# Kernel optimization log

Hardware: AMD Instinct MI355X
Metric: run time of the kernel (lower is better)

Reference implementation:

```python
import jax, jax.numpy as jnp
import numpy as np

ID, HD, B, T = 128, 256, 512, 128
MAX_REAL = 64
CAT_SEGS = [(64, 72), (72, 88), (88, 128)]
OUT_DIM = 128  # max index_end


def _lstm_scan(x, Wi, bi, Wh, bh):
    # x: [B, T, ID] -> hidden states [B, T, HD]
    b = x.shape[0]
    hd = Wh.shape[0]

    def step(carry, xt):
        h, c = carry
        gates = xt @ Wi + bi + h @ Wh + bh  # [B, 4*HD]
        f, i, a, o = jnp.split(gates, 4, axis=-1)
        f = jax.nn.sigmoid(f)
        i = jax.nn.sigmoid(i)
        a = jnp.tanh(a)
        o = jax.nn.sigmoid(o)
        c = f * c + i * a
        h = o * jnp.tanh(c)
        return (h, c), h

    init = (jnp.zeros((b, hd), x.dtype), jnp.zeros((b, hd), x.dtype))
    _, hs = jax.lax.scan(step, init, jnp.swapaxes(x, 0, 1))  # hs: [T, B, HD]
    return jnp.swapaxes(hs, 0, 1)


def setup_inputs() -> dict:
    key = jax.random.key(0)
    ks = jax.random.split(key, 16)
    s = 0.05
    inp = {
        "x0": jax.random.normal(ks[0], (B, T, ID), jnp.float32),
        "Wi_f": jax.random.normal(ks[1], (ID, 4 * HD), jnp.float32) * s,
        "bi_f": jnp.zeros((4 * HD,), jnp.float32),
        "Wh_f": jax.random.normal(ks[2], (HD, 4 * HD), jnp.float32) * s,
        "bh_f": jnp.zeros((4 * HD,), jnp.float32),
        "Wi_r": jax.random.normal(ks[3], (ID, 4 * HD), jnp.float32) * s,
        "bi_r": jnp.zeros((4 * HD,), jnp.float32),
        "Wh_r": jax.random.normal(ks[4], (HD, 4 * HD), jnp.float32) * s,
        "bh_r": jnp.zeros((4 * HD,), jnp.float32),
        "W1": jax.random.normal(ks[5], (2 * HD, HD), jnp.float32) * s,
        "b1": jnp.zeros((HD,), jnp.float32),
        "W2": jax.random.normal(ks[6], (HD, HD), jnp.float32) * s,
        "b2": jnp.zeros((HD,), jnp.float32),
        "W3": jax.random.normal(ks[7], (HD, OUT_DIM), jnp.float32) * s,
        "b3": jnp.zeros((OUT_DIM,), jnp.float32),
    }
    return inp


def reference(x0, Wi_f, bi_f, Wh_f, bh_f, Wi_r, bi_r, Wh_r, bh_r, W1, b1, W2, b2, W3, b3):
    x1_f = _lstm_scan(x0, Wi_f, bi_f, Wh_f, bh_f)            # [B, T, HD]
    x1_r = _lstm_scan(x0[:, ::-1, :], Wi_r, bi_r, Wh_r, bh_r) # [B, T, HD] (not flipped back, as in torch code)
    x1 = jnp.concatenate([x1_f, x1_r], axis=2)                # [B, T, 2*HD]
    x2 = jax.nn.leaky_relu(x1 @ W1 + b1, 0.1)
    x3 = jax.nn.leaky_relu(x2 @ W2 + b2, 0.1)
    x4 = x3 @ W3 + b3                                         # [B, T, OUT_DIM]
    parts = [jax.nn.sigmoid(x4[..., 0:MAX_REAL])]
    for s0, s1 in CAT_SEGS:
        parts.append(jax.nn.softmax(x4[..., s0:s1], axis=-1))
    return jnp.concatenate(parts, axis=-1)
```

## Files before the change

kernel.cpp:

```cpp
#include <hip/hip_runtime.h>

typedef unsigned short u16;
typedef unsigned long long u64;
typedef unsigned u32x4_t __attribute__((ext_vector_type(4)));
typedef _Float16 f16x8_t __attribute__((ext_vector_type(8)));
typedef short    i16x8_t __attribute__((ext_vector_type(8)));
typedef float    f32x4_t __attribute__((ext_vector_type(4)));

#define PIN(x) asm volatile("" : "+v"(x))

static __device__ __forceinline__ u16 f2h(float f) {
  _Float16 h = (_Float16)f;
  return __builtin_bit_cast(u16, h);
}
static __device__ __forceinline__ f32x4_t mfma16h(i16x8_t a, i16x8_t b, f32x4_t c) {
  return __builtin_amdgcn_mfma_f32_16x16x32_f16(
      __builtin_bit_cast(f16x8_t, a), __builtin_bit_cast(f16x8_t, b), c, 0, 0, 0);
}
static __device__ __forceinline__ float sigmoidf_(float x) { return 1.f / (1.f + __expf(-x)); }
static __device__ __forceinline__ float tanhf_(float x) { return 1.f - 2.f / (__expf(2.f * x) + 1.f); }

static __device__ __forceinline__ bool no_sent(u64 v) {
  u64 x = v ^ 0x7FFF7FFF7FFF7FFFull;
  return (((x - 0x0001000100010001ull) & ~x & 0x8000800080008000ull) == 0);
}
static __device__ __forceinline__ bool ok16(u32x4_t v) {
  u64 a = ((u64)v[1] << 32) | v[0];
  u64 b = ((u64)v[3] << 32) | v[2];
  return no_sent(a) && no_sent(b);
}

static __device__ __forceinline__ u32x4_t llc_load16(const u32x4_t* p) {
  u32x4_t r;
  asm volatile("global_load_dwordx4 %0, %1, off sc0 sc1\n\t"
               "s_waitcnt vmcnt(0)"
               : "=&v"(r) : "v"(p) : "memory");
  return r;
}
static __device__ __forceinline__ void llc_store4(unsigned* p, unsigned v) {
  asm volatile("global_store_dword %0, %1, off sc0 sc1" :: "v"(p), "v"(v) : "memory");
}

__global__ __launch_bounds__(256) void prep_all(
    const float* __restrict__ Wi_f, const float* __restrict__ Wh_f,
    const float* __restrict__ Wi_r, const float* __restrict__ Wh_r,
    const float* __restrict__ W1, const float* __restrict__ W2,
    const float* __restrict__ W3, u16* __restrict__ wpack,
    u16* __restrict__ w1t, u16* __restrict__ w2t, u16* __restrict__ w3t,
    uint4* __restrict__ x1v) {
  int b = blockIdx.x;
  if (b < 8192) {
    size_t id = (size_t)b * 256 + threadIdx.x;
    const uint4 s = {0x7FFF7FFFu, 0x7FFF7FFFu, 0x7FFF7FFFu, 0x7FFF7FFFu};
    x1v[id * 2] = s;
    x1v[id * 2 + 1] = s;
    return;
  }
  if (b < 11264) {
    int id = (b - 8192) * 256 + threadIdx.x;
    if (id >= 786432) return;
    int e = id & 7, r = id >> 3;
    int lane = r & 63; r >>= 6;
    int kb = r % 12; r /= 12;
    int tau = r & 63, dir = r >> 6;
    int mrow = lane & 15, quad = lane >> 4;
    int jb = tau >> 2, g = tau & 3;
    int n = g * 256 + jb * 16 + mrow;
    int k = kb * 32 + quad * 8 + e;
    const float* Wi = dir ? Wi_r : Wi_f;
    const float* Wh = dir ? Wh_r : Wh_f;
    float v = (k < 128) ? Wi[k * 1024 + n] : Wh[(k - 128) * 1024 + n];
    wpack[id] = f2h(v);
    return;
  }
  int id = (b - 11264) * 256 + threadIdx.x;
  if (id < 131072) { int n = id >> 9, k = id & 511; w1t[id] = f2h(W1[k * 256 + n]); return; }
  id -= 131072;
  if (id < 65536) { int n = id >> 8, k = id & 255; w2t[id] = f2h(W2[k * 256 + n]); return; }
  id -= 65536;
  if (id < 32768) { int n = id >> 8, k = id & 255; w3t[id] = f2h(W3[k * 128 + n]); }
}

__global__ __launch_bounds__(512, 2) void lstm_kernel(
    const float* __restrict__ x0, const u16* __restrict__ wpack,
    const float* __restrict__ bi_f, const float* __restrict__ bh_f,
    const float* __restrict__ bi_r, const float* __restrict__ bh_r,
    u16* __restrict__ x1) {
  __shared__ __align__(16) u16 lwh[16][8][64][8];
  __shared__ __align__(16) u16 ah[16][256];
  __shared__ __align__(16) float gbuf[16][260];

  const int tid = threadIdx.x;
  const int lane = tid & 63;
  const int w = tid >> 6;
  const int bid = blockIdx.x;
  const int q = bid >> 6;
  const int rem = bid & 63;
  const int dir = rem >> 5;
  const int grp = rem & 31;
  const int b0 = grp * 16;
  const u16* wpk = wpack + (size_t)dir * (64 * 12 * 64 * 8);
  const float* bi = dir ? bi_r : bi_f;
  const float* bh = dir ? bh_r : bh_f;
  const int mrow = lane & 15, quad = lane >> 4;
  const int tauL0 = 2 * w;

  float bias2[2];
#pragma unroll
  for (int lt = 0; lt < 2; ++lt) {
    int tau_g = 16 * q + tauL0 + lt;
    int n = (tau_g & 3) * 256 + (tau_g >> 2) * 16 + mrow;
    bias2[lt] = bi[n] + bh[n];
  }

#pragma unroll
  for (int r = 0; r < 16; ++r) {
    int d = r * 512 + tid;
    int ltau = d >> 9, lkb = (d >> 6) & 7, ll = d & 63;
    *(i16x8_t*)&lwh[ltau][lkb][ll][0] =
        *(const i16x8_t*)(wpk + (((size_t)(16 * q + ltau) * 12 + 4 + lkb) * 64 + ll) * 8);
  }
  i16x8_t wir[2][4];
#pragma unroll
  for (int lt = 0; lt < 2; ++lt)
#pragma unroll
    for (int kb = 0; kb < 4; ++kb) {
      wir[lt][kb] =
          *(const i16x8_t*)(wpk + (((size_t)(16 * q + tauL0 + lt) * 12 + kb) * 64 + lane) * 8);
      PIN(wir[lt][kb]);
    }
  __syncthreads();

  const int crow = tid >> 5;
  const int cj0 = (tid & 31) * 2;
  float c0 = 0.f, c1 = 0.f;

  const float* xfrag_base = x0 + (size_t)(b0 + mrow) * 16384 + quad * 8;
  const int fm = tid >> 5, fj = (tid & 31) * 8;
  const u16* hstage_src = x1 + (size_t)(b0 + fm) * 65536 + dir * 256 + fj;
  u16* ah_dst = &ah[fm][fj ^ ((fm & 7) << 3)];

  for (int t = 0; t < 128; ++t) {
    const int teff = dir ? 127 - t : t;

    i16x8_t afx[4];
    {
      const float* xp = xfrag_base + (size_t)teff * 128;
#pragma unroll
      for (int kb = 0; kb < 4; ++kb) {
        float4 va = *(const float4*)(xp + kb * 32);
        float4 vb = *(const float4*)(xp + kb * 32 + 4);
        i16x8_t v;
        v[0] = (short)f2h(va.x); v[1] = (short)f2h(va.y);
        v[2] = (short)f2h(va.z); v[3] = (short)f2h(va.w);
        v[4] = (short)f2h(vb.x); v[5] = (short)f2h(vb.y);
        v[6] = (short)f2h(vb.z); v[7] = (short)f2h(vb.w);
        afx[kb] = v;
      }
    }
    f32x4_t acc[2];
#pragma unroll
    for (int lt = 0; lt < 2; ++lt) {
      float bv = bias2[lt];
      f32x4_t a = {bv, bv, bv, bv};
      a = mfma16h(afx[0], wir[lt][0], a);
      a = mfma16h(afx[1], wir[lt][1], a);
      a = mfma16h(afx[2], wir[lt][2], a);
      a = mfma16h(afx[3], wir[lt][3], a);
      acc[lt] = a;
    }

    if (t > 0) {
      const u32x4_t* hsrc = (const u32x4_t*)(hstage_src + (size_t)(t - 1) * 512);
      u32x4_t hv4 = llc_load16(hsrc);
      unsigned iter = 0;
      while (!ok16(hv4)) {
        __builtin_amdgcn_s_sleep(1);
        hv4 = llc_load16(hsrc);
        if (++iter > (1u << 20)) break;
      }
      *(u32x4_t*)ah_dst = hv4;
    }
    __syncthreads();

    if (t > 0) {
      i16x8_t afh[8];
#pragma unroll
      for (int kb = 0; kb < 8; ++kb)
        afh[kb] = *(const i16x8_t*)&ah[mrow][(kb * 32 + quad * 8) ^ ((mrow & 7) << 3)];
#pragma unroll
      for (int lt = 0; lt < 2; ++lt) {
#pragma unroll
        for (int kb = 0; kb < 8; ++kb)
          acc[lt] = mfma16h(afh[kb], *(const i16x8_t*)&lwh[tauL0 + lt][kb][lane][0], acc[lt]);
      }
    }
#pragma unroll
    for (int lt = 0; lt < 2; ++lt) {
      int col = (tauL0 + lt) * 16 + mrow;
#pragma unroll
      for (int r = 0; r < 4; ++r) gbuf[quad * 4 + r][col] = acc[lt][r];
    }
    __syncthreads();

    {
      float hv[2];
#pragma unroll
      for (int e = 0; e < 2; ++e) {
        int jj = cj0 + e;
        int base = (jj >> 4) * 64 + (jj & 15);
        float fg = gbuf[crow][base];
        float ig = gbuf[crow][base + 16];
        float ag = gbuf[crow][base + 32];
        float og = gbuf[crow][base + 48];
        float cc = e ? c1 : c0;
        float cv = sigmoidf_(fg) * cc + sigmoidf_(ig) * tanhf_(ag);
        if (e) c1 = cv; else c0 = cv;
        hv[e] = sigmoidf_(og) * tanhf_(cv);
      }
      unsigned pack = (unsigned)f2h(hv[0]) | ((unsigned)f2h(hv[1]) << 16);
      unsigned* hp = (unsigned*)(x1 + ((size_t)((b0 + crow) * 128 + t)) * 512 +
                                 dir * 256 + 64 * q + cj0);
      llc_store4(hp, pack);
    }
  }
}

__global__ __launch_bounds__(512, 1) void mlp_kernel(
    const u16* __restrict__ x1, const u16* __restrict__ w1t,
    const u16* __restrict__ w2t, const u16* __restrict__ w3t,
    const float* __restrict__ b1, const float* __restrict__ b2,
    const float* __restrict__ b3, float* __restrict__ out) {
  __shared__ __align__(16) u16 xa[64][520];
  __shared__ __align__(16) u16 X2[64][264];
  __shared__ __align__(16) u16 X3[64][264];
  const int tid = threadIdx.x;
  const int lane = tid & 63;
  const int wv = tid >> 6;
  const int mrow = lane & 15, quad = lane >> 4;
  const int r0 = blockIdx.x * 64;
  const f32x4_t zero4 = {0.f, 0.f, 0.f, 0.f};

#pragma unroll
  for (int i = 0; i < 8; ++i) {
    int idx = i * 512 + tid;
    int row = idx >> 6, ch = idx & 63;
    *(i16x8_t*)&xa[row][ch * 8] =
        *(const i16x8_t*)(x1 + (size_t)(r0 + row) * 512 + ch * 8);
  }
  __syncthreads();

  {
    f32x4_t acc[2][4];
#pragma unroll
    for (int n = 0; n < 2; ++n)
#pragma unroll
      for (int rg = 0; rg < 4; ++rg) acc[n][rg] = zero4;
    for (int kb = 0; kb < 16; ++kb) {
      int k = kb * 32 + quad * 8;
      i16x8_t bf0 = *(const i16x8_t*)(w1t + ((wv * 2 + 0) * 16 + mrow) * 512 + k);
      i16x8_t bf1 = *(const i16x8_t*)(w1t + ((wv * 2 + 1) * 16 + mrow) * 512 + k);
#pragma unroll
      for (int rg = 0; rg < 4; ++rg) {
        i16x8_t a = *(const i16x8_t*)&xa[rg * 16 + mrow][k];
        acc[0][rg] = mfma16h(a, bf0, acc[0][rg]);
        acc[1][rg] = mfma16h(a, bf1, acc[1][rg]);
      }
    }
#pragma unroll
    for (int n = 0; n < 2; ++n)
#pragma unroll
      for (int rg = 0; rg < 4; ++rg)
#pragma unroll
        for (int r = 0; r < 4; ++r) {
          int m = rg * 16 + quad * 4 + r;
          int col = (wv * 2 + n) * 16 + mrow;
          float v = acc[n][rg][r] + b1[col];
          v = v > 0.f ? v : 0.1f * v;
          X2[m][col] = f2h(v);
        }
  }
  __syncthreads();

  {
    f32x4_t acc[2][4];
#pragma unroll
    for (int n = 0; n < 2; ++n)
#pragma unroll
      for (int rg = 0; rg < 4; ++rg) acc[n][rg] = zero4;
#pragma unroll
    for (int kb = 0; kb < 8; ++kb) {
      int k = kb * 32 + quad * 8;
      i16x8_t bf0 = *(const i16x8_t*)(w2t + ((wv * 2 + 0) * 16 + mrow) * 256 + k);
      i16x8_t bf1 = *(const i16x8_t*)(w2t + ((wv * 2 + 1) * 16 + mrow) * 256 + k);
#pragma unroll
      for (int rg = 0; rg < 4; ++rg) {
        i16x8_t a = *(const i16x8_t*)&X2[rg * 16 + mrow][k];
        acc[0][rg] = mfma16h(a, bf0, acc[0][rg]);
        acc[1][rg] = mfma16h(a, bf1, acc[1][rg]);
      }
    }
#pragma unroll
    for (int n = 0; n < 2; ++n)
#pragma unroll
      for (int rg = 0; rg < 4; ++rg)
#pragma unroll
        for (int r = 0; r < 4; ++r) {
          int m = rg * 16 + quad * 4 + r;
          int col = (wv * 2 + n) * 16 + mrow;
          float v = acc[n][rg][r] + b2[col];
          v = v > 0.f ? v : 0.1f * v;
          X3[m][col] = f2h(v);
        }
  }
  __syncthreads();

  float (*XF)[130] = (float (*)[130]) & X2[0][0];
  {
    f32x4_t acc[4];
#pragma unroll
    for (int rg = 0; rg < 4; ++rg) acc[rg] = zero4;
#pragma unroll
    for (int kb = 0; kb < 8; ++kb) {
      int k = kb * 32 + quad * 8;
      i16x8_t bf = *(const i16x8_t*)(w3t + (wv * 16 + mrow) * 256 + k);
#pragma unroll
      for (int rg = 0; rg < 4; ++rg) {
        i16x8_t a = *(const i16x8_t*)&X3[rg * 16 + mrow][k];
        acc[rg] = mfma16h(a, bf, acc[rg]);
      }
    }
#pragma unroll
    for (int rg = 0; rg < 4; ++rg)
#pragma unroll
      for (int r = 0; r < 4; ++r) {
        int m = rg * 16 + quad * 4 + r;
        int col = wv * 16 + mrow;
        XF[m][col] = acc[rg][r] + b3[col];
      }
  }
  __syncthreads();

  for (int i = 0; i < 8; ++i) {
    int idx = tid * 8 + i;
    int row = idx >> 6, cc = idx & 63;
    out[(size_t)(r0 + row) * 128 + cc] = sigmoidf_(XF[row][cc]);
  }
  if (tid < 192) {
    int row = tid / 3;
    int s = tid % 3;
    const int s0s[3] = {64, 72, 88};
    const int s1s[3] = {72, 88, 128};
    int s0 = s0s[s], s1 = s1s[s];
    float* xr = XF[row];
    float* op = out + (size_t)(r0 + row) * 128;
    float mx = xr[s0];
    for (int qq = s0 + 1; qq < s1; ++qq) mx = fmaxf(mx, xr[qq]);
    float sum = 0.f;
    for (int qq = s0; qq < s1; ++qq) { float e = __expf(xr[qq] - mx); xr[qq] = e; sum += e; }
    float inv = 1.f / sum;
    for (int qq = s0; qq < s1; ++qq) op[qq] = xr[qq] * inv;
  }
}

extern "C" void kernel_launch(void* const* d_in, const int* in_sizes, int n_in,
                              void* d_out, int out_size, void* d_ws, size_t ws_size,
                              hipStream_t stream) {
  const float* x0   = (const float*)d_in[0];
  const float* Wi_f = (const float*)d_in[1];
  const float* bi_f = (const float*)d_in[2];
  const float* Wh_f = (const float*)d_in[3];
  const float* bh_f = (const float*)d_in[4];
  const float* Wi_r = (const float*)d_in[5];
  const float* bi_r = (const float*)d_in[6];
  const float* Wh_r = (const float*)d_in[7];
  const float* bh_r = (const float*)d_in[8];
  const float* W1 = (const float*)d_in[9];
  const float* b1 = (const float*)d_in[10];
  const float* W2 = (const float*)d_in[11];
  const float* b2 = (const float*)d_in[12];
  const float* W3 = (const float*)d_in[13];
  const float* b3 = (const float*)d_in[14];
  float* out = (float*)d_out;

  char* ws = (char*)d_ws;
  u16* w1t   = (u16*)(ws + 0);
  u16* w2t   = (u16*)(ws + 262144);
  u16* w3t   = (u16*)(ws + 393216);
  u16* wpack = (u16*)(ws + 458752);
  u16* x1    = (u16*)(ws + 2031616);

  hipLaunchKernelGGL(prep_all, dim3(12160), dim3(256), 0, stream,
                     Wi_f, Wh_f, Wi_r, Wh_r, W1, W2, W3,
                     wpack, w1t, w2t, w3t, (uint4*)x1);
  hipLaunchKernelGGL(lstm_kernel, dim3(256), dim3(512), 0, stream,
                     x0, wpack, bi_f, bh_f, bi_r, bh_r, x1);
  hipLaunchKernelGGL(mlp_kernel, dim3(1024), dim3(512), 0, stream,
                     x1, w1t, w2t, w3t, b1, b2, b3, out);
}
```

Measured before the change: 547.1 us.

## Compute LSTM cell update in registers by assigning all four gates per wave

Each wave now computes the f, i, a and o gate tiles for one 16-column hidden slice, using 4 waves of 256 threads instead of 8. The cell update then runs directly on the MFMA accumulators, so the gbuf shared-memory round trip and the second per-step __syncthreads are gone. The h staging buffer is double-buffered by step parity so that one barrier per step suffices. In exchange each thread issues more MFMAs and holds more weight registers, and h is written with 2-byte scattered stores instead of 4-byte packed ones, which adds more cross-block polling traffic.

Result: no change. 537.7 us (median of 2 runs) (-1.7%).

```diff
diff --git a/kernel.cpp b/kernel.cpp
--- a/kernel.cpp
+++ b/kernel.cpp
@@ -37,8 +37,8 @@
                : "=&v"(r) : "v"(p) : "memory");
   return r;
 }
-static __device__ __forceinline__ void llc_store4(unsigned* p, unsigned v) {
-  asm volatile("global_store_dword %0, %1, off sc0 sc1" :: "v"(p), "v"(v) : "memory");
+static __device__ __forceinline__ void llc_store2(u16* p, unsigned v) {
+  asm volatile("global_store_short %0, %1, off sc0 sc1" :: "v"(p), "v"(v) : "memory");
 }
 
 __global__ __launch_bounds__(256) void prep_all(
@@ -81,14 +81,13 @@
   if (id < 32768) { int n = id >> 8, k = id & 255; w3t[id] = f2h(W3[k * 128 + n]); }
 }
 
-__global__ __launch_bounds__(512, 2) void lstm_kernel(
+__global__ __launch_bounds__(256, 1) void lstm_kernel(
     const float* __restrict__ x0, const u16* __restrict__ wpack,
     const float* __restrict__ bi_f, const float* __restrict__ bh_f,
     const float* __restrict__ bi_r, const float* __restrict__ bh_r,
     u16* __restrict__ x1) {
   __shared__ __align__(16) u16 lwh[16][8][64][8];
-  __shared__ __align__(16) u16 ah[16][256];
-  __shared__ __align__(16) float gbuf[16][260];
+  __shared__ __align__(16) u16 ah[2][16][256];
 
   const int tid = threadIdx.x;
   const int lane = tid & 63;
@@ -103,45 +102,45 @@
   const float* bi = dir ? bi_r : bi_f;
   const float* bh = dir ? bh_r : bh_f;
   const int mrow = lane & 15, quad = lane >> 4;
-  const int tauL0 = 2 * w;
-
-  float bias2[2];
-#pragma unroll
-  for (int lt = 0; lt < 2; ++lt) {
-    int tau_g = 16 * q + tauL0 + lt;
-    int n = (tau_g & 3) * 256 + (tau_g >> 2) * 16 + mrow;
-    bias2[lt] = bi[n] + bh[n];
-  }
-
-#pragma unroll
-  for (int r = 0; r < 16; ++r) {
-    int d = r * 512 + tid;
+  const int tauL0 = 4 * w;
+
+  float bias4[4];
+#pragma unroll
+  for (int g = 0; g < 4; ++g) {
+    int n = g * 256 + (4 * q + w) * 16 + mrow;
+    bias4[g] = bi[n] + bh[n];
+  }
+
+#pragma unroll
+  for (int r = 0; r < 32; ++r) {
+    int d = r * 256 + tid;
     int ltau = d >> 9, lkb = (d >> 6) & 7, ll = d & 63;
     *(i16x8_t*)&lwh[ltau][lkb][ll][0] =
         *(const i16x8_t*)(wpk + (((size_t)(16 * q + ltau) * 12 + 4 + lkb) * 64 + ll) * 8);
   }
-  i16x8_t wir[2][4];
-#pragma unroll
-  for (int lt = 0; lt < 2; ++lt)
+  i16x8_t wir[4][4];
+#pragma unroll
+  for (int g = 0; g < 4; ++g)
 #pragma unroll
     for (int kb = 0; kb < 4; ++kb) {
-      wir[lt][kb] =
-          *(const i16x8_t*)(wpk + (((size_t)(16 * q + tauL0 + lt) * 12 + kb) * 64 + lane) * 8);
-      PIN(wir[lt][kb]);
-    }
-  __syncthreads();
-
-  const int crow = tid >> 5;
-  const int cj0 = (tid & 31) * 2;
-  float c0 = 0.f, c1 = 0.f;
+      wir[g][kb] =
+          *(const i16x8_t*)(wpk + (((size_t)(16 * q + tauL0 + g) * 12 + kb) * 64 + lane) * 8);
+      PIN(wir[g][kb]);
+    }
+  for (int i = tid; i < 2 * 16 * 256; i += 256) ((u16*)ah)[i] = 0;
+  __syncthreads();
+
+  float c4[4] = {};
 
   const float* xfrag_base = x0 + (size_t)(b0 + mrow) * 16384 + quad * 8;
-  const int fm = tid >> 5, fj = (tid & 31) * 8;
+  const int fm = tid >> 4, fj = (tid & 15) * 16;
+  const int swz = (fm & 7) << 3;
   const u16* hstage_src = x1 + (size_t)(b0 + fm) * 65536 + dir * 256 + fj;
-  u16* ah_dst = &ah[fm][fj ^ ((fm & 7) << 3)];
+  u16* hstore_base = x1 + (size_t)(b0 + quad * 4) * 65536 + dir * 256 + 64 * q + w * 16 + mrow;
 
   for (int t = 0; t < 128; ++t) {
     const int teff = dir ? 127 - t : t;
+    const int par = t & 1;
 
     i16x8_t afx[4];
     {
@@ -158,28 +157,32 @@
         afx[kb] = v;
       }
     }
-    f32x4_t acc[2];
-#pragma unroll
-    for (int lt = 0; lt < 2; ++lt) {
-      float bv = bias2[lt];
+    f32x4_t acc[4];
+#pragma unroll
+    for (int g = 0; g < 4; ++g) {
+      float bv = bias4[g];
       f32x4_t a = {bv, bv, bv, bv};
-      a = mfma16h(afx[0], wir[lt][0], a);
-      a = mfma16h(afx[1], wir[lt][1], a);
-      a = mfma16h(afx[2], wir[lt][2], a);
-      a = mfma16h(afx[3], wir[lt][3], a);
-      acc[lt] = a;
+      a = mfma16h(afx[0], wir[g][0], a);
+      a = mfma16h(afx[1], wir[g][1], a);
+      a = mfma16h(afx[2], wir[g][2], a);
+      a = mfma16h(afx[3], wir[g][3], a);
+      acc[g] = a;
     }
 
     if (t > 0) {
       const u32x4_t* hsrc = (const u32x4_t*)(hstage_src + (size_t)(t - 1) * 512);
-      u32x4_t hv4 = llc_load16(hsrc);
+      u32x4_t h0 = llc_load16(hsrc);
+      u32x4_t h1 = llc_load16(hsrc + 1);
       unsigned iter = 0;
-      while (!ok16(hv4)) {
+      while (!(ok16(h0) && ok16(h1))) {
         __builtin_amdgcn_s_sleep(1);
-        hv4 = llc_load16(hsrc);
+        if (!ok16(h0)) h0 = llc_load16(hsrc);
+        if (!ok16(h1)) h1 = llc_load16(hsrc + 1);
         if (++iter > (1u << 20)) break;
       }
-      *(u32x4_t*)ah_dst = hv4;
+      u16* abase = &ah[par][0][0];
+      *(u32x4_t*)(abase + fm * 256 + (fj ^ swz)) = h0;
+      *(u32x4_t*)(abase + fm * 256 + ((fj + 8) ^ swz)) = h1;
     }
     __syncthreads();
 
@@ -187,41 +190,25 @@
       i16x8_t afh[8];
 #pragma unroll
       for (int kb = 0; kb < 8; ++kb)
-        afh[kb] = *(const i16x8_t*)&ah[mrow][(kb * 32 + quad * 8) ^ ((mrow & 7) << 3)];
-#pragma unroll
-      for (int lt = 0; lt < 2; ++lt) {
+        afh[kb] = *(const i16x8_t*)&ah[par][mrow][(kb * 32 + quad * 8) ^ ((mrow & 7) << 3)];
+#pragma unroll
+      for (int g = 0; g < 4; ++g) {
 #pragma unroll
         for (int kb = 0; kb < 8; ++kb)
-          acc[lt] = mfma16h(afh[kb], *(const i16x8_t*)&lwh[tauL0 + lt][kb][lane][0], acc[lt]);
-      }
-    }
-#pragma unroll
-    for (int lt = 0; lt < 2; ++lt) {
-      int col = (tauL0 + lt) * 16 + mrow;
-#pragma unroll
-      for (int r = 0; r < 4; ++r) gbuf[quad * 4 + r][col] = acc[lt][r];
-    }
-    __syncthreads();
-
-    {
-      float hv[2];
-#pragma unroll
-      for (int e = 0; e < 2; ++e) {
-        int jj = cj0 + e;
-        int base = (jj >> 4) * 64 + (jj & 15);
-        float fg = gbuf[crow][base];
-        float ig = gbuf[crow][base + 16];
-        float ag = gbuf[crow][base + 32];
-        float og = gbuf[crow][base + 48];
-        float cc = e ? c1 : c0;
-        float cv = sigmoidf_(fg) * cc + sigmoidf_(ig) * tanhf_(ag);
-        if (e) c1 = cv; else c0 = cv;
-        hv[e] = sigmoidf_(og) * tanhf_(cv);
-      }
-      unsigned pack = (unsigned)f2h(hv[0]) | ((unsigned)f2h(hv[1]) << 16);
-      unsigned* hp = (unsigned*)(x1 + ((size_t)((b0 + crow) * 128 + t)) * 512 +
-                                 dir * 256 + 64 * q + cj0);
-      llc_store4(hp, pack);
+          acc[g] = mfma16h(afh[kb], *(const i16x8_t*)&lwh[tauL0 + g][kb][lane][0], acc[g]);
+      }
+    }
+
+#pragma unroll
+    for (int r = 0; r < 4; ++r) {
+      float fv = sigmoidf_(acc[0][r]);
+      float iv = sigmoidf_(acc[1][r]);
+      float av = tanhf_(acc[2][r]);
+      float ov = sigmoidf_(acc[3][r]);
+      float cv = fv * c4[r] + iv * av;
+      c4[r] = cv;
+      float hv = ov * tanhf_(cv);
+      llc_store2(hstore_base + ((size_t)r * 128 + t) * 512, (unsigned)f2h(hv));
     }
   }
 }
@@ -393,7 +380,7 @@
   hipLaunchKernelGGL(prep_all, dim3(12160), dim3(256), 0, stream,
                      Wi_f, Wh_f, Wi_r, Wh_r, W1, W2, W3,
                      wpack, w1t, w2t, w3t, (uint4*)x1);
-  hipLaunchKernelGGL(lstm_kernel, dim3(256), dim3(512), 0, stream,
+  hipLaunchKernelGGL(lstm_kernel, dim3(256), dim3(256), 0, stream,
                      x0, wpack, bi_f, bh_f, bi_r, bh_r, x1);
   hipLaunchKernelGGL(mlp_kernel, dim3(1024), dim3(512), 0, stream,
                      x1, w1t, w2t, w3t, b1, b2, b3, out);
```
